# Optimization experiments

Hardware: AMD Instinct MI355X
Metric: run time of the kernel (lower is better)

Reference implementation:

```python
import jax, jax.numpy as jnp
import numpy as np

N_EMBED = 1024
N_HEAD = 16
HEAD_DIM = N_EMBED // N_HEAD


def setup_inputs() -> dict:
    key = jax.random.key(0)
    k1, k2, k3, k4, k5 = jax.random.split(key, 5)
    x = jax.random.normal(k1, (4, 2048, N_EMBED), dtype=jnp.float32)
    s = 1.0 / np.sqrt(N_EMBED)
    W_attn = jax.random.normal(k2, (N_EMBED, 3 * N_EMBED), dtype=jnp.float32) * s
    b_attn = jnp.zeros((3 * N_EMBED,), dtype=jnp.float32)
    W_proj = jax.random.normal(k3, (N_EMBED, N_EMBED), dtype=jnp.float32) * s
    b_proj = jnp.zeros((N_EMBED,), dtype=jnp.float32)
    return {"x": x, "W_attn": W_attn, "b_attn": b_attn, "W_proj": W_proj, "b_proj": b_proj}


def reference(x, W_attn, b_attn, W_proj, b_proj):
    B, T, C = x.shape
    qkv = x @ W_attn + b_attn  # [B, T, 3C]
    q, k, v = jnp.split(qkv, 3, axis=2)
    # [B, H, T, D]
    q = q.reshape(B, T, N_HEAD, HEAD_DIM).transpose(0, 2, 1, 3)
    k = k.reshape(B, T, N_HEAD, HEAD_DIM).transpose(0, 2, 1, 3)
    v = v.reshape(B, T, N_HEAD, HEAD_DIM).transpose(0, 2, 1, 3)
    scale = 1.0 / np.sqrt(HEAD_DIM)
    scores = jnp.einsum('bhqd,bhkd->bhqk', q, k) * scale
    causal = jnp.tril(jnp.ones((T, T), dtype=bool))
    scores = jnp.where(causal[None, None], scores, -jnp.inf)
    attn = jax.nn.softmax(scores, axis=-1)
    y = jnp.einsum('bhqk,bhkd->bhqd', attn, v)
    y = y.transpose(0, 2, 1, 3).reshape(B, T, C)
    return y @ W_proj + b_proj
```

## Files before the change

### kernel.cpp

```cpp
#include <hip/hip_runtime.h>

typedef unsigned short u16;
typedef unsigned int u32;
typedef unsigned long long u64;
typedef __attribute__((ext_vector_type(8))) __bf16 b8;
typedef __attribute__((ext_vector_type(4))) float f32x4;

#define T_SEQ 2048
#define NB 4
#define NH 16
#define HD 64
#define CEMB 1024
#define M_ROWS (NB * T_SEQ)
#define Q_PRESCALE 0.18033688011112042f

__device__ __forceinline__ u16 f2bf(float f) {
  union { float f; unsigned int u; } v; v.f = f;
  unsigned int r = v.u + 0x7FFFu + ((v.u >> 16) & 1u);
  return (u16)(r >> 16);
}

__device__ __forceinline__ u32 pk2bf(float a, float b) {
  __bf16 x = (__bf16)a, y = (__bf16)b;
  return (u32)*(u16*)&x | ((u32)*(u16*)&y << 16);
}

__device__ __forceinline__ void gl_lds16(const u16* g, u16* l) {
  __builtin_amdgcn_global_load_lds(
      (const __attribute__((address_space(1))) unsigned int*)g,
      (__attribute__((address_space(3))) unsigned int*)l, 16, 0, 0);
}

#define BARRIER() __builtin_amdgcn_s_barrier()
#define LGKM0() do { asm volatile("s_waitcnt lgkmcnt(0)" ::: "memory"); \
                     __builtin_amdgcn_sched_barrier(0); } while (0)
#define VMCNT4() asm volatile("s_waitcnt vmcnt(4)" ::: "memory")
#define VMCNT2() asm volatile("s_waitcnt vmcnt(2)" ::: "memory")
#define VMCNT0() asm volatile("s_waitcnt vmcnt(0)" ::: "memory")

__global__ __launch_bounds__(256) void k_prepass(const float* __restrict__ x,
                                                 u16* __restrict__ x_bf,
                                                 const float* __restrict__ W_attn,
                                                 u16* __restrict__ wattn_t,
                                                 const float* __restrict__ W_proj,
                                                 u16* __restrict__ wproj_t) {
  __shared__ u16 t[64][65];
  const int bidx = blockIdx.x;
  if (bidx < 2048) {
    const int n4 = (NB * T_SEQ * CEMB) / 4;
    const int stride = 2048 * 256;
    for (int i = bidx * 256 + threadIdx.x; i < n4; i += stride) {
      float4 v = ((const float4*)x)[i];
      ushort4 o;
      o.x = f2bf(v.x); o.y = f2bf(v.y); o.z = f2bf(v.z); o.w = f2bf(v.w);
      ((ushort4*)x_bf)[i] = o;
    }
  } else {
    const float* W; u16* Wt; int N, tloc;
    if (bidx < 2816) { W = W_attn; Wt = wattn_t; N = 3 * CEMB; tloc = bidx - 2048; }
    else             { W = W_proj; Wt = wproj_t; N = CEMB;     tloc = bidx - 2816; }
    const int K = CEMB;
    const int nx = N / 64;
    const int k0 = (tloc / nx) * 64, n0 = (tloc % nx) * 64;
    const int tx = threadIdx.x & 63, ty = threadIdx.x >> 6;
    for (int i = ty; i < 64; i += 4)
      t[i][tx] = f2bf(W[(size_t)(k0 + i) * N + n0 + tx]);
    __syncthreads();
    for (int i = ty; i < 64; i += 4)
      Wt[(size_t)(n0 + i) * K + k0 + tx] = t[tx][i];
  }
}

template <int MODE, int BNU>
__global__ __launch_bounds__(512, 2) void k_gemm8(const u16* __restrict__ A,
                                                  const u16* __restrict__ Bt,
                                                  const float* __restrict__ bias,
                                                  u16* __restrict__ out_bf,
                                                  float* __restrict__ out_f,
                                                  u16* __restrict__ vt,
                                                  int M, int N, int K, int mstripe) {
  __shared__ u16 sA[2][16384];
  __shared__ u16 sB[2][BNU * 4096];
  constexpr int NI = BNU / 2;
  const int tid = threadIdx.x;
  const int lane = tid & 63;
  const int wid = tid >> 6;
  const int wm = wid >> 2;
  const int wn = wid & 3;
  const int fr = lane & 15;
  const int g = lane >> 4;

  const int xcd = blockIdx.x & 7;
  const int idx = blockIdx.x >> 3;
  const int mt = xcd * mstripe + (idx % mstripe);
  const int nt = idx / mstripe;
  const int row0 = mt * 256, col0 = nt * (BNU * 64);
  const int NT = K >> 6;

  const int kswz = ((lane & 7) ^ ((lane >> 3) & 7)) * 8;
  const u16* gA = A + (size_t)(row0 + wid * 8 + (lane >> 3)) * K + kswz;
  const u16* gB = Bt + (size_t)(col0 + wid * 8 + (lane >> 3)) * K + kswz;

#define SGA(buf, T, u) gl_lds16(gA + (size_t)(u) * 64 * K + (size_t)(T) * 64, \
                                &sA[buf][(u) * 4096 + wid * 512])
#define SGB(buf, T, u) gl_lds16(gB + (size_t)(u) * 64 * K + (size_t)(T) * 64, \
                                &sB[buf][(u) * 4096 + wid * 512])
#define RDA(dst, rowe, ks)                                                     \
  { int row_ = (rowe);                                                         \
    dst = *(const b8*)&sA[bufc][row_ * 64 + ((((ks)*4 + g) ^ (row_ & 7)) << 3)]; }
#define RDB(dst, cole, ks)                                                     \
  { int col_ = (cole);                                                         \
    dst = *(const b8*)&sB[bufc][col_ * 64 + ((((ks)*4 + g) ^ (col_ & 7)) << 3)]; }

  f32x4 acc[8][BNU] = {};
  b8 aF[4][2], bF0[NI][2], bF1[NI][2];

#pragma unroll
  for (int u = 0; u < BNU; ++u) SGB(0, 0, u);
  SGA(0, 0, 0); SGA(0, 0, 2);
  SGA(0, 0, 1); SGA(0, 0, 3);
  SGA(1, 1, 0); SGA(1, 1, 2);
  VMCNT4();
  BARRIER();
  __builtin_amdgcn_sched_barrier(0);

#pragma unroll 2
  for (int T = 0; T < NT; ++T) {
    const int bufc = T & 1, bufn = bufc ^ 1;
    const bool st1 = (T + 1 < NT), st2 = (T + 2 < NT);

#pragma unroll
    for (int mi = 0; mi < 4; ++mi)
#pragma unroll
      for (int ks = 0; ks < 2; ++ks) RDA(aF[mi][ks], wm * 128 + mi * 16 + fr, ks);
#pragma unroll
    for (int ni = 0; ni < NI; ++ni)
#pragma unroll
      for (int ks = 0; ks < 2; ++ks) RDB(bF0[ni][ks], wn * (BNU * 16) + ni * 16 + fr, ks);
    if (st1) { SGB(bufn, T + 1, 0); SGB(bufn, T + 1, 1); }
    else VMCNT0();
    BARRIER(); LGKM0();
    __builtin_amdgcn_s_setprio(1);
#pragma unroll
    for (int mi = 0; mi < 4; ++mi)
#pragma unroll
      for (int ni = 0; ni < NI; ++ni)
#pragma unroll
        for (int ks = 0; ks < 2; ++ks)
          acc[mi][ni] = __builtin_amdgcn_mfma_f32_16x16x32_bf16(aF[mi][ks], bF0[ni][ks], acc[mi][ni], 0, 0, 0);
    __builtin_amdgcn_s_setprio(0);
    __builtin_amdgcn_sched_barrier(0);
    BARRIER();

#pragma unroll
    for (int ni = 0; ni < NI; ++ni)
#pragma unroll
      for (int ks = 0; ks < 2; ++ks) RDB(bF1[ni][ks], wn * (BNU * 16) + (NI + ni) * 16 + fr, ks);
    if (BNU == 4 && st1) { SGB(bufn, T + 1, 2); SGB(bufn, T + 1, 3); }
    if constexpr (BNU == 4) { VMCNT4(); } else { VMCNT2(); }
    BARRIER(); LGKM0();
    __builtin_amdgcn_s_setprio(1);
#pragma unroll
    for (int mi = 0; mi < 4; ++mi)
#pragma unroll
      for (int ni = 0; ni < NI; ++ni)
#pragma unroll
        for (int ks = 0; ks < 2; ++ks)
          acc[mi][NI + ni] = __builtin_amdgcn_mfma_f32_16x16x32_bf16(aF[mi][ks], bF1[ni][ks], acc[mi][NI + ni], 0, 0, 0);
    __builtin_amdgcn_s_setprio(0);
    __builtin_amdgcn_sched_barrier(0);
    BARRIER();

#pragma unroll
    for (int mi = 0; mi < 4; ++mi)
#pragma unroll
      for (int ks = 0; ks < 2; ++ks) RDA(aF[mi][ks], wm * 128 + 64 + mi * 16 + fr, ks);
    if (st2) { SGA(bufc, T + 2, 0); SGA(bufc, T + 2, 2); }
    BARRIER(); LGKM0();
    __builtin_amdgcn_s_setprio(1);
#pragma unroll
    for (int mi = 0; mi < 4; ++mi)
#pragma unroll
      for (int ni = 0; ni < NI; ++ni)
#pragma unroll
        for (int ks = 0; ks < 2; ++ks)
          acc[4 + mi][ni] = __builtin_amdgcn_mfma_f32_16x16x32_bf16(aF[mi][ks], bF0[ni][ks], acc[4 + mi][ni], 0, 0, 0);
    __builtin_amdgcn_s_setprio(0);
    __builtin_amdgcn_sched_barrier(0);
    BARRIER();

    if (st1) { SGA(bufn, T + 1, 1); SGA(bufn, T + 1, 3); }
    VMCNT4();
    BARRIER();
    __builtin_amdgcn_sched_barrier(0);
    __builtin_amdgcn_s_setprio(1);
#pragma unroll
    for (int mi = 0; mi < 4; ++mi)
#pragma unroll
      for (int ni = 0; ni < NI; ++ni)
#pragma unroll
        for (int ks = 0; ks < 2; ++ks)
          acc[4 + mi][NI + ni] = __builtin_amdgcn_mfma_f32_16x16x32_bf16(aF[mi][ks], bF1[ni][ks], acc[4 + mi][NI + ni], 0, 0, 0);
    __builtin_amdgcn_s_setprio(0);
    __builtin_amdgcn_sched_barrier(0);
    BARRIER();
  }
#undef SGA
#undef SGB
#undef RDA
#undef RDB

  const int fg = lane >> 4;
  if (MODE != 2) {
#pragma unroll
    for (int ni = 0; ni < BNU; ++ni) {
      int col = col0 + wn * (BNU * 16) + ni * 16 + fr;
      float bv = bias[col];
#pragma unroll
      for (int mi = 0; mi < 8; ++mi) {
#pragma unroll
        for (int r = 0; r < 4; ++r) {
          int row = row0 + wm * 128 + mi * 16 + fg * 4 + r;
          float v = acc[mi][ni][r] + bv;
          if (MODE == 0) {
            float sc = (col < CEMB) ? Q_PRESCALE : 1.0f;
            out_bf[(size_t)row * (2 * CEMB) + col] = f2bf(v * sc);
          } else {
            out_f[(size_t)row * N + col] = v;
          }
        }
      }
    }
  } else {
    u16* st = (u16*)sA;
    const int bq = row0 >> 11;
    const int t0g = row0 & (T_SEQ - 1);
#pragma unroll
    for (int pass = 0; pass < 2; ++pass) {
      __syncthreads();
      if ((wn >> 1) == pass) {
#pragma unroll
        for (int nn = 0; nn < BNU; ++nn) {
          const int hdl = (wn & 1) * 32 + nn * 16 + fr;
          const float bv = bias[col0 + pass * 64 + hdl];
#pragma unroll
          for (int mi = 0; mi < 8; ++mi) {
            const int tl = wm * 128 + mi * 16 + fg * 4;
#pragma unroll
            for (int rp = 0; rp < 2; ++rp) {
              u32 pk = pk2bf(acc[mi][nn][2 * rp] + bv, acc[mi][nn][2 * rp + 1] + bv);
              *(u32*)&st[hdl * 280 + tl + 2 * rp] = pk;
            }
          }
        }
      }
      __syncthreads();
      const int hd_r = tid >> 3;
      const int ck = tid & 7;
      u16* vrow = vt + ((size_t)(bq * (NH * HD) + col0 + pass * 64 + hd_r)) * T_SEQ + t0g;
#pragma unroll
      for (int j = 0; j < 4; ++j) {
        const int chunk = ck + 8 * j;
        f32x4 d = *(const f32x4*)&st[hd_r * 280 + chunk * 8];
        *(f32x4*)&vrow[chunk * 8] = d;
      }
    }
  }
}

__global__ __launch_bounds__(256, 4) void k_attn(const u16* __restrict__ qk,
                                                 const u16* __restrict__ vtg,
                                                 u16* __restrict__ y) {
  __shared__ __align__(16) u16 kt_s[2][64 * 64];
  __shared__ __align__(16) u16 vt_s[2][64 * 64];
  __shared__ __align__(16) char pl_s[4][2048];

  const int lane = threadIdx.x & 63;
  const int wave = threadIdx.x >> 6;
  const int tid = threadIdx.x;
  const int g = lane >> 4, c = lane & 15;

  const int xcd = blockIdx.x & 7;
  const int idx = blockIdx.x >> 3;
  const int bh = xcd * 8 + (idx & 7);
  const int pr = idx >> 3;
  const int b = bh >> 4, h = bh & 15;

  char* plw = pl_s[wave];
  char* plA = plw + c * 128;
  const int b3 = c >> 3;
  const int e2 = (c & 7) << 1;
  const int sb = g + b3 * 8;

  b8 ones_frag;
#pragma unroll
  for (int e = 0; e < 8; ++e) ones_frag[e] = (c == 0) ? (__bf16)1.0f : (__bf16)0.0f;

  const int srow = tid >> 3;
  const int scc = (tid & 7) ^ (srow & 7);
  const u16* ksrc0 = qk + ((size_t)(b * T_SEQ) + srow) * (2 * CEMB) + CEMB + h * HD + scc * 8;
  const u16* vsrc0 = vtg + ((size_t)(bh * HD) + srow) * T_SEQ + scc * 8;

#define STAGE(t, bb)                                                    \
  {                                                                     \
    const u16* ks_ = ksrc0 + (size_t)(t) * 64 * (2 * CEMB);             \
    const u16* vs_ = vsrc0 + (t) * 64;                                  \
    gl_lds16(ks_, &kt_s[bb][wave * 512]);                               \
    gl_lds16(ks_ + 32 * (2 * CEMB), &kt_s[bb][wave * 512 + 2048]);      \
    gl_lds16(vs_, &vt_s[bb][wave * 512]);                               \
    gl_lds16(vs_ + 32 * T_SEQ, &vt_s[bb][wave * 512 + 2048]);           \
  }

#pragma unroll 1
  for (int seg = 0; seg < 2; ++seg) {
    const int tt = seg ? pr : (31 - pr);
    const int qW = tt * 64 + wave * 16;

    const u16* qrow = qk + (size_t)(b * T_SEQ + qW + c) * (2 * CEMB) + h * HD + g * 8;
    const b8 qf0 = *(const b8*)qrow;
    const b8 qf1 = *(const b8*)(qrow + 32);

    float m = -3e38f;
    f32x4 o[4] = {};
    f32x4 o4 = {0.f, 0.f, 0.f, 0.f};

    const int ntt = tt + 1;
    int cur = 0;
    STAGE(0, 0);
    __syncthreads();

    for (int t = 0; t < ntt; ++t) {
      if (t + 1 < ntt) STAGE(t + 1, cur ^ 1);
      const int k0 = t * 64;
      const bool diag = (t == ntt - 1);
      const u16* kt = kt_s[cur];
      const u16* vtl = vt_s[cur];

      f32x4 s[4] = {{0.f,0.f,0.f,0.f},{0.f,0.f,0.f,0.f},{0.f,0.f,0.f,0.f},{0.f,0.f,0.f,0.f}};
      __builtin_amdgcn_s_setprio(1);
#pragma unroll
      for (int n = 0; n < 4; ++n) {
        if (!diag || n <= wave) {
          const b8 kf0 = *(const b8*)&kt[(n * 16 + c) * 64 + ((g ^ (c & 7)) << 3)];
          const b8 kf1 = *(const b8*)&kt[(n * 16 + c) * 64 + (((4 + g) ^ (c & 7)) << 3)];
          s[n] = __builtin_amdgcn_mfma_f32_16x16x32_bf16(kf0, qf0, s[n], 0, 0, 0);
          s[n] = __builtin_amdgcn_mfma_f32_16x16x32_bf16(kf1, qf1, s[n], 0, 0, 0);
        }
      }
      __builtin_amdgcn_s_setprio(0);

      if (diag) {
#pragma unroll
        for (int n = 0; n < 4; ++n)
#pragma unroll
          for (int r = 0; r < 4; ++r)
            if (k0 + n * 16 + g * 4 + r > qW + c) s[n][r] = -3e38f;
      }

      float rm = fmaxf(fmaxf(fmaxf(s[0][0], s[0][1]), s[0][2]),
                       fmaxf(fmaxf(s[0][3], s[1][0]), s[1][1]));
      rm = fmaxf(rm, fmaxf(fmaxf(s[1][2], s[1][3]), s[2][0]));
      rm = fmaxf(rm, fmaxf(fmaxf(s[2][1], s[2][2]), s[2][3]));
      rm = fmaxf(rm, fmaxf(fmaxf(s[3][0], s[3][1]), fmaxf(s[3][2], s[3][3])));
      rm = fmaxf(rm, __shfl_xor(rm, 16));
      rm = fmaxf(rm, __shfl_xor(rm, 32));

      if (!__all(rm <= m + 8.0f)) {
        float mn = fmaxf(m, rm);
        float al = __builtin_amdgcn_exp2f(m - mn);
        m = mn;
#pragma unroll
        for (int r = 0; r < 4; ++r) {
          int src = (lane & 48) + g * 4 + r;
          float a = __shfl(al, src);
#pragma unroll
          for (int nt = 0; nt < 4; ++nt) o[nt][r] *= a;
          o4[r] *= a;
        }
      }

#pragma unroll
      for (int n = 0; n < 4; ++n) {
        u32 lo = pk2bf(__builtin_amdgcn_exp2f(s[n][0] - m),
                       __builtin_amdgcn_exp2f(s[n][1] - m));
        u32 hi = pk2bf(__builtin_amdgcn_exp2f(s[n][2] - m),
                       __builtin_amdgcn_exp2f(s[n][3] - m));
        *(u64*)(plA + ((((4 * n + sb) & 15) ^ e2) << 3)) = ((u64)hi << 32) | lo;
      }

      b8 vb[2][4];
#pragma unroll
      for (int ks = 0; ks < 2; ++ks)
#pragma unroll
        for (int nt = 0; nt < 4; ++nt)
          vb[ks][nt] = *(const b8*)&vtl[(nt * 16 + c) * 64 + (((ks * 4 + g) ^ (c & 7)) << 3)];

      __builtin_amdgcn_s_setprio(1);
#pragma unroll
      for (int ks = 0; ks < 2; ++ks) {
        const b8 pa = *(const b8*)(plA + ((((ks * 8 + 2 * g + 8 * b3) & 15) ^ e2) << 3));
        o4 = __builtin_amdgcn_mfma_f32_16x16x32_bf16(pa, ones_frag, o4, 0, 0, 0);
#pragma unroll
        for (int nt = 0; nt < 4; ++nt)
          o[nt] = __builtin_amdgcn_mfma_f32_16x16x32_bf16(pa, vb[ks][nt], o[nt], 0, 0, 0);
      }
      __builtin_amdgcn_s_setprio(0);

      __syncthreads();
      cur ^= 1;
    }

#pragma unroll
    for (int r = 0; r < 4; ++r) {
      float lr = __shfl(o4[r], lane & 48);
      float inv = 1.0f / lr;
#pragma unroll
      for (int nt = 0; nt < 4; ++nt) {
        __bf16 ov = (__bf16)(o[nt][r] * inv);
        y[(size_t)(b * T_SEQ + qW + g * 4 + r) * CEMB + h * HD + nt * 16 + c] = *(u16*)&ov;
      }
    }
  }
#undef STAGE
}

extern "C" void kernel_launch(void* const* d_in, const int* in_sizes, int n_in,
                              void* d_out, int out_size, void* d_ws, size_t ws_size,
                              hipStream_t stream) {
  const float* x = (const float*)d_in[0];
  const float* W_attn = (const float*)d_in[1];
  const float* b_attn = (const float*)d_in[2];
  const float* W_proj = (const float*)d_in[3];
  const float* b_proj = (const float*)d_in[4];
  float* out = (float*)d_out;

  char* ws = (char*)d_ws;
  u16* x_bf    = (u16*)(ws);
  u16* wattn_t = (u16*)(ws + 16777216);
  u16* wproj_t = (u16*)(ws + 23068672);
  u16* qk_bf   = (u16*)(ws + 25165824);
  u16* vt      = (u16*)(ws + 58720256);
  u16* y_bf    = (u16*)(ws + 75497472);

  k_prepass<<<3072, 256, 0, stream>>>(x, x_bf, W_attn, wattn_t, W_proj, wproj_t);
  k_gemm8<0, 4><<<256, 512, 0, stream>>>(x_bf, wattn_t, b_attn, qk_bf, nullptr, nullptr,
                                         M_ROWS, 2 * CEMB, CEMB, 4);
  k_gemm8<2, 2><<<256, 512, 0, stream>>>(x_bf, wattn_t + 2048 * CEMB, b_attn + 2 * CEMB,
                                         nullptr, nullptr, vt, M_ROWS, CEMB, CEMB, 4);
  k_attn<<<1024, 256, 0, stream>>>(qk_bf, vt, y_bf);
  k_gemm8<1, 2><<<256, 512, 0, stream>>>(y_bf, wproj_t, b_proj, nullptr, out, nullptr,
                                         M_ROWS, CEMB, CEMB, 4);
}
```

Before: 179.8 us.

## Split attention tile softmax and PV MFMA into two halves for overlap

```diff
diff --git a/kernel.cpp b/kernel.cpp
--- a/kernel.cpp
+++ b/kernel.cpp
@@ -349,6 +349,13 @@
       }
       __builtin_amdgcn_s_setprio(0);
 
+      b8 vb[2][4];
+#pragma unroll
+      for (int ks = 0; ks < 2; ++ks)
+#pragma unroll
+        for (int nt = 0; nt < 4; ++nt)
+          vb[ks][nt] = *(const b8*)&vtl[(nt * 16 + c) * 64 + (((ks * 4 + g) ^ (c & 7)) << 3)];
+
       if (diag) {
 #pragma unroll
         for (int n = 0; n < 4; ++n)
@@ -357,16 +364,17 @@
             if (k0 + n * 16 + g * 4 + r > qW + c) s[n][r] = -3e38f;
       }
 
-      float rm = fmaxf(fmaxf(fmaxf(s[0][0], s[0][1]), s[0][2]),
-                       fmaxf(fmaxf(s[0][3], s[1][0]), s[1][1]));
-      rm = fmaxf(rm, fmaxf(fmaxf(s[1][2], s[1][3]), s[2][0]));
-      rm = fmaxf(rm, fmaxf(fmaxf(s[2][1], s[2][2]), s[2][3]));
-      rm = fmaxf(rm, fmaxf(fmaxf(s[3][0], s[3][1]), fmaxf(s[3][2], s[3][3])));
-      rm = fmaxf(rm, __shfl_xor(rm, 16));
-      rm = fmaxf(rm, __shfl_xor(rm, 32));
-
-      if (!__all(rm <= m + 8.0f)) {
-        float mn = fmaxf(m, rm);
+      float rm0 = fmaxf(fmaxf(fmaxf(s[0][0], s[0][1]), fmaxf(s[0][2], s[0][3])),
+                        fmaxf(fmaxf(s[1][0], s[1][1]), fmaxf(s[1][2], s[1][3])));
+      rm0 = fmaxf(rm0, __shfl_xor(rm0, 16));
+      rm0 = fmaxf(rm0, __shfl_xor(rm0, 32));
+      float rm1 = fmaxf(fmaxf(fmaxf(s[2][0], s[2][1]), fmaxf(s[2][2], s[2][3])),
+                        fmaxf(fmaxf(s[3][0], s[3][1]), fmaxf(s[3][2], s[3][3])));
+      rm1 = fmaxf(rm1, __shfl_xor(rm1, 16));
+      rm1 = fmaxf(rm1, __shfl_xor(rm1, 32));
+
+      if (!__all(rm0 <= m + 8.0f)) {
+        float mn = fmaxf(m, rm0);
         float al = __builtin_amdgcn_exp2f(m - mn);
         m = mn;
 #pragma unroll
@@ -378,9 +386,8 @@
           o4[r] *= a;
         }
       }
-
-#pragma unroll
-      for (int n = 0; n < 4; ++n) {
+#pragma unroll
+      for (int n = 0; n < 2; ++n) {
         u32 lo = pk2bf(__builtin_amdgcn_exp2f(s[n][0] - m),
                        __builtin_amdgcn_exp2f(s[n][1] - m));
         u32 hi = pk2bf(__builtin_amdgcn_exp2f(s[n][2] - m),
@@ -388,21 +395,45 @@
         *(u64*)(plA + ((((4 * n + sb) & 15) ^ e2) << 3)) = ((u64)hi << 32) | lo;
       }
 
-      b8 vb[2][4];
-#pragma unroll
-      for (int ks = 0; ks < 2; ++ks)
+      __builtin_amdgcn_s_setprio(1);
+      {
+        const b8 pa = *(const b8*)(plA + ((((2 * g + 8 * b3) & 15) ^ e2) << 3));
+        o4 = __builtin_amdgcn_mfma_f32_16x16x32_bf16(pa, ones_frag, o4, 0, 0, 0);
 #pragma unroll
         for (int nt = 0; nt < 4; ++nt)
-          vb[ks][nt] = *(const b8*)&vtl[(nt * 16 + c) * 64 + (((ks * 4 + g) ^ (c & 7)) << 3)];
+          o[nt] = __builtin_amdgcn_mfma_f32_16x16x32_bf16(pa, vb[0][nt], o[nt], 0, 0, 0);
+      }
+      __builtin_amdgcn_s_setprio(0);
+
+      if (!__all(rm1 <= m + 8.0f)) {
+        float mn = fmaxf(m, rm1);
+        float al = __builtin_amdgcn_exp2f(m - mn);
+        m = mn;
+#pragma unroll
+        for (int r = 0; r < 4; ++r) {
+          int src = (lane & 48) + g * 4 + r;
+          float a = __shfl(al, src);
+#pragma unroll
+          for (int nt = 0; nt < 4; ++nt) o[nt][r] *= a;
+          o4[r] *= a;
+        }
+      }
+#pragma unroll
+      for (int n = 2; n < 4; ++n) {
+        u32 lo = pk2bf(__builtin_amdgcn_exp2f(s[n][0] - m),
+                       __builtin_amdgcn_exp2f(s[n][1] - m));
+        u32 hi = pk2bf(__builtin_amdgcn_exp2f(s[n][2] - m),
+                       __builtin_amdgcn_exp2f(s[n][3] - m));
+        *(u64*)(plA + ((((4 * n + sb) & 15) ^ e2) << 3)) = ((u64)hi << 32) | lo;
+      }
 
       __builtin_amdgcn_s_setprio(1);
-#pragma unroll
-      for (int ks = 0; ks < 2; ++ks) {
-        const b8 pa = *(const b8*)(plA + ((((ks * 8 + 2 * g + 8 * b3) & 15) ^ e2) << 3));
+      {
+        const b8 pa = *(const b8*)(plA + ((((8 + 2 * g + 8 * b3) & 15) ^ e2) << 3));
         o4 = __builtin_amdgcn_mfma_f32_16x16x32_bf16(pa, ones_frag, o4, 0, 0, 0);
 #pragma unroll
         for (int nt = 0; nt < 4; ++nt)
-          o[nt] = __builtin_amdgcn_mfma_f32_16x16x32_bf16(pa, vb[ks][nt], o[nt], 0, 0, 0);
+          o[nt] = __builtin_amdgcn_mfma_f32_16x16x32_bf16(pa, vb[1][nt], o[nt], 0, 0, 0);
       }
       __builtin_amdgcn_s_setprio(0);
 
```

After: 184.4 us. 1.03x slower.
